# Performance work log

Measured on AMD Instinct MI355X. Metric: run time of the kernel, lower is better.

The kernel has to match this reference:

```python
import jax, jax.numpy as jnp
import numpy as np

D = 768       # input embedding dim
H = 256       # hidden_dim
NH = 4        # num_heads
HD = H // NH  # head_dim = 64
M = 131072    # number of candidate LLM embeddings


def setup_inputs() -> dict:
    key = jax.random.key(0)
    ks = jax.random.split(key, 16)
    s = 0.02
    return {
        "user": jax.random.normal(ks[0], (D,), jnp.float32),
        "query": jax.random.normal(ks[1], (D,), jnp.float32),
        "llm": jax.random.normal(ks[2], (M, D), jnp.float32),
        # projection weights (torch Linear: y = x @ W.T + b)
        "Wu": jax.random.normal(ks[3], (H, D), jnp.float32) * s,
        "bu": jnp.zeros((H,), jnp.float32),
        "Wq": jax.random.normal(ks[4], (H, D), jnp.float32) * s,
        "bq": jnp.zeros((H,), jnp.float32),
        "Wl": jax.random.normal(ks[5], (H, D), jnp.float32) * s,
        "bl": jnp.zeros((H,), jnp.float32),
        # MultiheadAttention packed in-projection [3H, H] and bias [3H]
        "in_proj_w": jax.random.normal(ks[6], (3 * H, H), jnp.float32) * s,
        "in_proj_b": jnp.zeros((3 * H,), jnp.float32),
        "out_proj_w": jax.random.normal(ks[7], (H, H), jnp.float32) * s,
        "out_proj_b": jnp.zeros((H,), jnp.float32),
        # final scoring linear: [1, 2H]
        "Wo": jax.random.normal(ks[8], (1, 2 * H), jnp.float32) * s,
        "bo": jnp.zeros((1,), jnp.float32),
    }


def reference(user, query, llm, Wu, bu, Wq, bq, Wl, bl,
              in_proj_w, in_proj_b, out_proj_w, out_proj_b, Wo, bo):
    m = llm.shape[0]
    # input projections
    u = user @ Wu.T + bu            # [H]
    qv = query @ Wq.T + bq          # [H]
    l = llm @ Wl.T + bl             # [M, H]
    # context rows are identical for every candidate -> compute K/V once on [2, H]
    ctx = jnp.stack([u, qv], axis=0)                      # [2, H]
    Wq_a, Wk_a, Wv_a = jnp.split(in_proj_w, 3, axis=0)    # each [H, H]
    bq_a, bk_a, bv_a = jnp.split(in_proj_b, 3, axis=0)
    q = (l @ Wq_a.T + bq_a).reshape(m, NH, HD)            # [M, nh, hd] (seq_len=1)
    k = (ctx @ Wk_a.T + bk_a).reshape(2, NH, HD)          # [2, nh, hd]
    v = (ctx @ Wv_a.T + bv_a).reshape(2, NH, HD)
    scale = 1.0 / jnp.sqrt(jnp.asarray(HD, q.dtype))
    scores = jnp.einsum('mhd,khd->mhk', q, k) * scale     # [M, nh, 2]
    attn = jax.nn.softmax(scores, axis=-1)
    attended = jnp.einsum('mhk,khd->mhd', attn, v).reshape(m, H)
    attended = attended @ out_proj_w.T + out_proj_b       # [M, H]
    x = jnp.concatenate([attended, l], axis=-1)           # [M, 2H]
    # out = Sequential(ReLU, Dropout(eval=identity), Linear(2H, 1))
    logits = (jax.nn.relu(x) @ Wo.T + bo).squeeze(-1)     # [M]
    return logits
```

## Files before the change

kernel.cpp:

```cpp
#include <hip/hip_runtime.h>


typedef float f32x4 __attribute__((ext_vector_type(4)));
typedef __bf16 bf16x8 __attribute__((ext_vector_type(8)));

#define VMCNT(n) asm volatile("s_waitcnt vmcnt(" #n ")" ::: "memory")

__device__ __forceinline__ unsigned f2bf(float f) {
  unsigned u = __builtin_bit_cast(unsigned, f);
  u += 0x7fffu + ((u >> 16) & 1u);
  return u >> 16;
}

__device__ __forceinline__ void gl_lds16(const void* g, void* l) {
  __builtin_amdgcn_global_load_lds(
      (const __attribute__((address_space(1))) void*)g,
      (__attribute__((address_space(3))) void*)l, 16, 0, 0);
}

__global__ void prep_a(const float* __restrict__ user, const float* __restrict__ query,
                       const float* __restrict__ Wu, const float* __restrict__ bu,
                       const float* __restrict__ Wq, const float* __restrict__ bq,
                       float* __restrict__ wf) {
  const int og = threadIdx.x >> 5, ln = threadIdx.x & 31;
  const int o = blockIdx.x * 8 + og;
  const int isq = o >> 8, j = o & 255;
  const float* Wrow = (isq ? Wq : Wu) + (size_t)j * 768;
  const float* vec = isq ? query : user;
  float p = 0.f;
  #pragma unroll
  for (int i = 0; i < 24; ++i) { int d = ln * 24 + i; p = fmaf(Wrow[d], vec[d], p); }
  #pragma unroll
  for (int off = 16; off; off >>= 1) p += __shfl_xor(p, off);
  if (ln == 0) wf[o] = p + (isq ? bq[j] : bu[j]);
}

__global__ void prep_b(const float* __restrict__ ipw, const float* __restrict__ ipb,
                       float* __restrict__ wf) {
  const int og = threadIdx.x >> 5, ln = threadIdx.x & 31;
  const int o = blockIdx.x * 8 + og;
  const int kv = o >> 9, cc = (o >> 8) & 1, j = o & 255;
  const int row = 256 + kv * 256 + j;
  const float* Wrow = ipw + (size_t)row * 256;
  const float* ctx = wf + cc * 256;
  float p = 0.f;
  #pragma unroll
  for (int i = 0; i < 8; ++i) { int d = ln * 8 + i; p = fmaf(Wrow[d], ctx[d], p); }
  #pragma unroll
  for (int off = 16; off; off >>= 1) p += __shfl_xor(p, off);
  if (ln == 0) wf[512 + o] = p + ipb[row];
}

__global__ void prep_c(const float* __restrict__ ipw, const float* __restrict__ ipb,
                       const float* __restrict__ opw, const float* __restrict__ opb,
                       float* __restrict__ wf) {
  const int t = threadIdx.x, b = blockIdx.x;
  if (b < 4) {
    const int h = b;
    float acc = 0.f;
    for (int d = 0; d < 64; ++d) {
      float kd = wf[512 + h * 64 + d] - wf[768 + h * 64 + d];
      acc = fmaf(ipw[(size_t)(h * 64 + d) * 256 + t], kd, acc);
    }
    wf[1536 + h * 256 + t] = 0.125f * acc;
    if (t == 0) {
      float cs = 0.f;
      for (int d = 0; d < 64; ++d)
        cs = fmaf(ipb[h * 64 + d], wf[512 + h * 64 + d] - wf[768 + h * 64 + d], cs);
      wf[3840 + h] = 0.125f * cs;
    }
  } else {
    const float* oprow = opw + (size_t)t * 256;
    float bse = 0.f;
    for (int i = 0; i < 256; ++i) bse = fmaf(oprow[i], wf[1280 + i], bse);
    wf[2560 + t] = bse + opb[t];
    #pragma unroll
    for (int h = 0; h < 4; ++h) {
      float dl = 0.f;
      for (int d = 0; d < 64; ++d)
        dl = fmaf(oprow[h * 64 + d], wf[1024 + h * 64 + d] - wf[1280 + h * 64 + d], dl);
      wf[2816 + h * 256 + t] = dl;
    }
  }
}

__global__ void prep_w(const float* __restrict__ Wl, unsigned int* __restrict__ Bs4) {
  const int tid = blockIdx.x * 256 + threadIdx.x;
  const int lane = tid & 63;
  const int ntk = tid >> 6;
  const int kk = ntk >> 4, nt = ntk & 15;
  const int k = kk * 32 + (lane >> 4) * 8;
  const int j = nt * 16 + (lane & 15);
  const float* src = Wl + (size_t)j * 768 + k;
  uint4 pk;
  pk.x = f2bf(src[0]) | (f2bf(src[1]) << 16);
  pk.y = f2bf(src[2]) | (f2bf(src[3]) << 16);
  pk.z = f2bf(src[4]) | (f2bf(src[5]) << 16);
  pk.w = f2bf(src[6]) | (f2bf(src[7]) << 16);
  ((uint4*)Bs4)[tid] = pk;
}

__global__ __launch_bounds__(512, 2) void fused_main(
    const float* __restrict__ llm, const float* __restrict__ bl,
    const float* __restrict__ Wo, const float* __restrict__ bo,
    const float* __restrict__ wf, float* __restrict__ out) {

  __shared__ __align__(16) char smem[131072];

  const int t = threadIdx.x;
  const int w = t >> 6, l = t & 63, g = l >> 4, c = l & 15;
  const int wr = w >> 1, wc = w & 1;
  const int m0 = blockIdx.x * 128;
  const char* BsB = (const char*)(wf + 4096);

  auto stage_pair = [&](int slot, int kk) {
    #pragma unroll
    for (int r = 0; r < 2; ++r) {
      const int chunk = r * 512 + w * 64 + l;
      const int row = chunk >> 3;
      const int cb = (chunk & 7) * 16;
      const int cl = cb ^ ((row & 7) << 4);
      const char* gp = (const char*)(llm + (size_t)(m0 + row) * 768 + kk * 32) + cl;
      gl_lds16(gp, smem + slot * 16384 + r * 8192 + w * 1024);
    }
    const char* gb = BsB + (size_t)kk * 16384;
    #pragma unroll
    for (int r = 0; r < 2; ++r) {
      const int chunk = r * 512 + w * 64 + l;
      gl_lds16(gb + (size_t)chunk * 16,
               smem + 65536 + slot * 16384 + r * 8192 + w * 1024);
    }
  };

  stage_pair(0, 0);
  stage_pair(1, 1);
  stage_pair(2, 2);

  f32x4 acc[2][8];
  #pragma unroll
  for (int rf = 0; rf < 2; ++rf)
    #pragma unroll
    for (int cf = 0; cf < 8; ++cf) acc[rf][cf] = (f32x4){0.f, 0.f, 0.f, 0.f};

  const int sx = (c & 7) << 4;

  #pragma unroll
  for (int kk = 0; kk < 24; ++kk) {
    if (kk < 22)      { VMCNT(8); }
    else if (kk == 22){ VMCNT(4); }
    else              { VMCNT(0); }
    __builtin_amdgcn_s_barrier();

    if (kk < 21) stage_pair((kk + 3) & 3, kk + 3);

    const char* ab = smem + (kk & 3) * 16384;
    const char* bb = smem + 65536 + (kk & 3) * 16384 + (size_t)wc * 8192 + l * 16;

    bf16x8 afr[2];
    #pragma unroll
    for (int rf = 0; rf < 2; ++rf) {
      const int row = wr * 32 + rf * 16 + c;
      const char* rp = ab + row * 128;
      const float4 fa = *(const float4*)(rp + ((g * 32) ^ sx));
      const float4 fb = *(const float4*)(rp + ((g * 32 + 16) ^ sx));
      uint4 pk;
      pk.x = f2bf(fa.x) | (f2bf(fa.y) << 16);
      pk.y = f2bf(fa.z) | (f2bf(fa.w) << 16);
      pk.z = f2bf(fb.x) | (f2bf(fb.y) << 16);
      pk.w = f2bf(fb.z) | (f2bf(fb.w) << 16);
      afr[rf] = __builtin_bit_cast(bf16x8, pk);
    }
    #pragma unroll
    for (int cf = 0; cf < 8; ++cf) {
      const bf16x8 bfr = *(const bf16x8*)(bb + cf * 1024);
      #pragma unroll
      for (int rf = 0; rf < 2; ++rf)
        acc[rf][cf] = __builtin_amdgcn_mfma_f32_16x16x32_bf16(
            afr[rf], bfr, acc[rf][cf], 0, 0, 0);
    }
  }

  __syncthreads();

  float* smf = (float*)smem;
  float* wsd_s  = smf;
  float* delta_s = smf + 1024;
  float* base_s = smf + 2048;
  float* woa_s  = smf + 2304;
  float* wo2_s  = smf + 2560;
  float* bl_s   = smf + 2816;
  float* psd_p  = smf + 3072;
  float* pr2_p  = smf + 4096;
  float* a_s    = smf + 4352;
  float* r2_s   = smf + 4864;
  float* p2_s   = smf + 4992;
  float* csd_s  = smf + 5504;
  for (int i = t; i < 1024; i += 512) { wsd_s[i] = wf[1536 + i]; delta_s[i] = wf[2816 + i]; }
  if (t < 256) {
    base_s[t] = wf[2560 + t];
    woa_s[t] = Wo[t];
    wo2_s[t] = Wo[256 + t];
    bl_s[t] = bl[t];
  }
  if (t < 4) csd_s[t] = wf[3840 + t];
  __syncthreads();

  #pragma unroll
  for (int rf = 0; rf < 2; ++rf) {
    float psd[4][4] = {};
    float pr2[4] = {};
    #pragma unroll
    for (int cf = 0; cf < 8; ++cf) {
      const int col = wc * 128 + cf * 16 + c;
      const float w0 = wsd_s[col], w1 = wsd_s[256 + col],
                  w2 = wsd_s[512 + col], w3 = wsd_s[768 + col];
      const float wo = wo2_s[col], bb2 = bl_s[col];
      #pragma unroll
      for (int j = 0; j < 4; ++j) {
        const float x = acc[rf][cf][j] + bb2;
        psd[j][0] = fmaf(x, w0, psd[j][0]);
        psd[j][1] = fmaf(x, w1, psd[j][1]);
        psd[j][2] = fmaf(x, w2, psd[j][2]);
        psd[j][3] = fmaf(x, w3, psd[j][3]);
        pr2[j] = fmaf(fmaxf(x, 0.f), wo, pr2[j]);
      }
    }
    #pragma unroll
    for (int off = 8; off; off >>= 1) {
      #pragma unroll
      for (int j = 0; j < 4; ++j) {
        #pragma unroll
        for (int h = 0; h < 4; ++h) psd[j][h] += __shfl_xor(psd[j][h], off);
        pr2[j] += __shfl_xor(pr2[j], off);
      }
    }
    if (c == 0) {
      #pragma unroll
      for (int j = 0; j < 4; ++j) {
        const int row = wr * 32 + rf * 16 + g * 4 + j;
        #pragma unroll
        for (int h = 0; h < 4; ++h) psd_p[wc * 512 + row * 4 + h] = psd[j][h];
        pr2_p[wc * 128 + row] = pr2[j];
      }
    }
  }
  __syncthreads();

  if (t < 128) {
    #pragma unroll
    for (int h = 0; h < 4; ++h) {
      const float sd = csd_s[h] + psd_p[t * 4 + h] + psd_p[512 + t * 4 + h];
      a_s[t * 4 + h] = 1.f / (1.f + __expf(-sd));
    }
    r2_s[t] = pr2_p[t] + pr2_p[128 + t];
  }
  __syncthreads();

  {
    const int r = t & 127, q = t >> 7;
    const float a0 = a_s[r * 4], a1 = a_s[r * 4 + 1],
                a2 = a_s[r * 4 + 2], a3 = a_s[r * 4 + 3];
    float p = 0.f;
    const int j0 = q * 64;
    #pragma unroll 4
    for (int j = j0; j < j0 + 64; ++j) {
      float att = base_s[j];
      att = fmaf(a0, delta_s[j], att);
      att = fmaf(a1, delta_s[256 + j], att);
      att = fmaf(a2, delta_s[512 + j], att);
      att = fmaf(a3, delta_s[768 + j], att);
      p = fmaf(fmaxf(att, 0.f), woa_s[j], p);
    }
    p2_s[q * 128 + r] = p;
  }
  __syncthreads();
  if (t < 128)
    out[m0 + t] = p2_s[t] + p2_s[128 + t] + p2_s[256 + t] + p2_s[384 + t]
                + r2_s[t] + bo[0];
}

extern "C" void kernel_launch(void* const* d_in, const int* in_sizes, int n_in,
                              void* d_out, int out_size, void* d_ws, size_t ws_size,
                              hipStream_t stream) {
  const float* user  = (const float*)d_in[0];
  const float* query = (const float*)d_in[1];
  const float* llm   = (const float*)d_in[2];
  const float* Wu    = (const float*)d_in[3];
  const float* bu    = (const float*)d_in[4];
  const float* Wq    = (const float*)d_in[5];
  const float* bq    = (const float*)d_in[6];
  const float* Wl    = (const float*)d_in[7];
  const float* bl    = (const float*)d_in[8];
  const float* ipw   = (const float*)d_in[9];
  const float* ipb   = (const float*)d_in[10];
  const float* opw   = (const float*)d_in[11];
  const float* opb   = (const float*)d_in[12];
  const float* Wo    = (const float*)d_in[13];
  const float* bo    = (const float*)d_in[14];
  float* out = (float*)d_out;
  float* wf = (float*)d_ws;
  unsigned int* Bs4 = (unsigned int*)(wf + 4096);

  prep_a<<<64, 256, 0, stream>>>(user, query, Wu, bu, Wq, bq, wf);
  prep_w<<<96, 256, 0, stream>>>(Wl, Bs4);
  prep_b<<<128, 256, 0, stream>>>(ipw, ipb, wf);
  prep_c<<<5, 256, 0, stream>>>(ipw, ipb, opw, opb, wf);
  fused_main<<<131072 / 128, 512, 0, stream>>>(llm, bl, Wo, bo, wf, out);
}
```

Baseline: 197.0 us.

## Merge prep kernels into one launch and shrink main-kernel pipeline to double buffering

Replaces the four small prep kernels with one 97-block kernel. One block computes all the context, K/V and out-projection precomputations serially, passing intermediates through shared memory, while the other blocks convert Wl to bf16. In the main GEMM kernel the 4-stage LDS pipeline becomes a 2-stage double buffer, halving LDS to 64KB so more blocks can be resident per CU. Launch bounds are raised and the k-loop unroll is dropped. The single-block prep does its dot products serially with row-strided loads and may be slow. The shallower pipeline exposes more load latency per block, in exchange for higher occupancy.

```diff
diff --git a/kernel.cpp b/kernel.cpp
--- a/kernel.cpp
+++ b/kernel.cpp
@@ -18,94 +18,86 @@
       (__attribute__((address_space(3))) void*)l, 16, 0, 0);
 }
 
-__global__ void prep_a(const float* __restrict__ user, const float* __restrict__ query,
-                       const float* __restrict__ Wu, const float* __restrict__ bu,
-                       const float* __restrict__ Wq, const float* __restrict__ bq,
-                       float* __restrict__ wf) {
-  const int og = threadIdx.x >> 5, ln = threadIdx.x & 31;
-  const int o = blockIdx.x * 8 + og;
-  const int isq = o >> 8, j = o & 255;
-  const float* Wrow = (isq ? Wq : Wu) + (size_t)j * 768;
-  const float* vec = isq ? query : user;
-  float p = 0.f;
-  #pragma unroll
-  for (int i = 0; i < 24; ++i) { int d = ln * 24 + i; p = fmaf(Wrow[d], vec[d], p); }
-  #pragma unroll
-  for (int off = 16; off; off >>= 1) p += __shfl_xor(p, off);
-  if (ln == 0) wf[o] = p + (isq ? bq[j] : bu[j]);
-}
-
-__global__ void prep_b(const float* __restrict__ ipw, const float* __restrict__ ipb,
-                       float* __restrict__ wf) {
-  const int og = threadIdx.x >> 5, ln = threadIdx.x & 31;
-  const int o = blockIdx.x * 8 + og;
-  const int kv = o >> 9, cc = (o >> 8) & 1, j = o & 255;
-  const int row = 256 + kv * 256 + j;
-  const float* Wrow = ipw + (size_t)row * 256;
-  const float* ctx = wf + cc * 256;
-  float p = 0.f;
-  #pragma unroll
-  for (int i = 0; i < 8; ++i) { int d = ln * 8 + i; p = fmaf(Wrow[d], ctx[d], p); }
-  #pragma unroll
-  for (int off = 16; off; off >>= 1) p += __shfl_xor(p, off);
-  if (ln == 0) wf[512 + o] = p + ipb[row];
-}
-
-__global__ void prep_c(const float* __restrict__ ipw, const float* __restrict__ ipb,
-                       const float* __restrict__ opw, const float* __restrict__ opb,
-                       float* __restrict__ wf) {
-  const int t = threadIdx.x, b = blockIdx.x;
-  if (b < 4) {
-    const int h = b;
+__global__ void prep_all(const float* __restrict__ user, const float* __restrict__ query,
+                         const float* __restrict__ Wu, const float* __restrict__ bu,
+                         const float* __restrict__ Wq, const float* __restrict__ bq,
+                         const float* __restrict__ Wl,
+                         const float* __restrict__ ipw, const float* __restrict__ ipb,
+                         const float* __restrict__ opw, const float* __restrict__ opb,
+                         float* __restrict__ wf, unsigned int* __restrict__ Bs4) {
+  const int t = threadIdx.x;
+  if (blockIdx.x < 96) {
+    const int tid = blockIdx.x * 256 + t;
+    const int lane = tid & 63;
+    const int ntk = tid >> 6;
+    const int kk = ntk >> 4, nt = ntk & 15;
+    const int k = kk * 32 + (lane >> 4) * 8;
+    const int j = nt * 16 + (lane & 15);
+    const float* src = Wl + (size_t)j * 768 + k;
+    uint4 pk;
+    pk.x = f2bf(src[0]) | (f2bf(src[1]) << 16);
+    pk.y = f2bf(src[2]) | (f2bf(src[3]) << 16);
+    pk.z = f2bf(src[4]) | (f2bf(src[5]) << 16);
+    pk.w = f2bf(src[6]) | (f2bf(src[7]) << 16);
+    ((uint4*)Bs4)[tid] = pk;
+    return;
+  }
+  __shared__ float sh[1536];
+  for (int o = t; o < 512; o += 256) {
+    const int isq = o >> 8, j = o & 255;
+    const float* Wrow = (isq ? Wq : Wu) + (size_t)j * 768;
+    const float* vec = isq ? query : user;
+    float p = 0.f;
+    for (int d = 0; d < 768; ++d) p = fmaf(Wrow[d], vec[d], p);
+    p += (isq ? bq[j] : bu[j]);
+    sh[o] = p; wf[o] = p;
+  }
+  __syncthreads();
+  for (int o = t; o < 1024; o += 256) {
+    const int kv = o >> 9, cc = (o >> 8) & 1, j = o & 255;
+    const int row = 256 + kv * 256 + j;
+    const float* Wrow = ipw + (size_t)row * 256;
+    const float* ctx = sh + cc * 256;
+    float p = 0.f;
+    for (int d = 0; d < 256; ++d) p = fmaf(Wrow[d], ctx[d], p);
+    p += ipb[row];
+    sh[512 + o] = p; wf[512 + o] = p;
+  }
+  __syncthreads();
+  #pragma unroll
+  for (int h = 0; h < 4; ++h) {
     float acc = 0.f;
     for (int d = 0; d < 64; ++d) {
-      float kd = wf[512 + h * 64 + d] - wf[768 + h * 64 + d];
+      const float kd = sh[512 + h * 64 + d] - sh[768 + h * 64 + d];
       acc = fmaf(ipw[(size_t)(h * 64 + d) * 256 + t], kd, acc);
     }
     wf[1536 + h * 256 + t] = 0.125f * acc;
-    if (t == 0) {
-      float cs = 0.f;
-      for (int d = 0; d < 64; ++d)
-        cs = fmaf(ipb[h * 64 + d], wf[512 + h * 64 + d] - wf[768 + h * 64 + d], cs);
-      wf[3840 + h] = 0.125f * cs;
-    }
-  } else {
-    const float* oprow = opw + (size_t)t * 256;
-    float bse = 0.f;
-    for (int i = 0; i < 256; ++i) bse = fmaf(oprow[i], wf[1280 + i], bse);
-    wf[2560 + t] = bse + opb[t];
-    #pragma unroll
-    for (int h = 0; h < 4; ++h) {
-      float dl = 0.f;
-      for (int d = 0; d < 64; ++d)
-        dl = fmaf(oprow[h * 64 + d], wf[1024 + h * 64 + d] - wf[1280 + h * 64 + d], dl);
-      wf[2816 + h * 256 + t] = dl;
-    }
-  }
-}
-
-__global__ void prep_w(const float* __restrict__ Wl, unsigned int* __restrict__ Bs4) {
-  const int tid = blockIdx.x * 256 + threadIdx.x;
-  const int lane = tid & 63;
-  const int ntk = tid >> 6;
-  const int kk = ntk >> 4, nt = ntk & 15;
-  const int k = kk * 32 + (lane >> 4) * 8;
-  const int j = nt * 16 + (lane & 15);
-  const float* src = Wl + (size_t)j * 768 + k;
-  uint4 pk;
-  pk.x = f2bf(src[0]) | (f2bf(src[1]) << 16);
-  pk.y = f2bf(src[2]) | (f2bf(src[3]) << 16);
-  pk.z = f2bf(src[4]) | (f2bf(src[5]) << 16);
-  pk.w = f2bf(src[6]) | (f2bf(src[7]) << 16);
-  ((uint4*)Bs4)[tid] = pk;
-}
-
-__global__ __launch_bounds__(512, 2) void fused_main(
+  }
+  if (t < 4) {
+    float cs = 0.f;
+    for (int d = 0; d < 64; ++d)
+      cs = fmaf(ipb[t * 64 + d], sh[512 + t * 64 + d] - sh[768 + t * 64 + d], cs);
+    wf[3840 + t] = 0.125f * cs;
+  }
+  const float* oprow = opw + (size_t)t * 256;
+  float bse = 0.f;
+  for (int i = 0; i < 256; ++i) bse = fmaf(oprow[i], sh[1280 + i], bse);
+  wf[2560 + t] = bse + opb[t];
+  #pragma unroll
+  for (int h = 0; h < 4; ++h) {
+    float dl = 0.f;
+    for (int d = 0; d < 64; ++d)
+      dl = fmaf(oprow[h * 64 + d], sh[1024 + h * 64 + d] - sh[1280 + h * 64 + d], dl);
+    wf[2816 + h * 256 + t] = dl;
+  }
+}
+
+__global__ __launch_bounds__(512, 4) void fused_main(
     const float* __restrict__ llm, const float* __restrict__ bl,
     const float* __restrict__ Wo, const float* __restrict__ bo,
     const float* __restrict__ wf, float* __restrict__ out) {
 
-  __shared__ __align__(16) char smem[131072];
+  __shared__ __align__(16) char smem[65536];
 
   const int t = threadIdx.x;
   const int w = t >> 6, l = t & 63, g = l >> 4, c = l & 15;
@@ -128,13 +120,11 @@
     for (int r = 0; r < 2; ++r) {
       const int chunk = r * 512 + w * 64 + l;
       gl_lds16(gb + (size_t)chunk * 16,
-               smem + 65536 + slot * 16384 + r * 8192 + w * 1024);
+               smem + 32768 + slot * 16384 + r * 8192 + w * 1024);
     }
   };
 
   stage_pair(0, 0);
-  stage_pair(1, 1);
-  stage_pair(2, 2);
 
   f32x4 acc[2][8];
   #pragma unroll
@@ -144,17 +134,13 @@
 
   const int sx = (c & 7) << 4;
 
-  #pragma unroll
   for (int kk = 0; kk < 24; ++kk) {
-    if (kk < 22)      { VMCNT(8); }
-    else if (kk == 22){ VMCNT(4); }
-    else              { VMCNT(0); }
     __builtin_amdgcn_s_barrier();
-
-    if (kk < 21) stage_pair((kk + 3) & 3, kk + 3);
-
-    const char* ab = smem + (kk & 3) * 16384;
-    const char* bb = smem + 65536 + (kk & 3) * 16384 + (size_t)wc * 8192 + l * 16;
+    if (kk < 23) { stage_pair((kk + 1) & 1, kk + 1); VMCNT(4); }
+    else         { VMCNT(0); }
+
+    const char* ab = smem + (kk & 1) * 16384;
+    const char* bb = smem + 32768 + (kk & 1) * 16384 + (size_t)wc * 8192 + l * 16;
 
     bf16x8 afr[2];
     #pragma unroll
@@ -301,9 +287,7 @@
   float* wf = (float*)d_ws;
   unsigned int* Bs4 = (unsigned int*)(wf + 4096);
 
-  prep_a<<<64, 256, 0, stream>>>(user, query, Wu, bu, Wq, bq, wf);
-  prep_w<<<96, 256, 0, stream>>>(Wl, Bs4);
-  prep_b<<<128, 256, 0, stream>>>(ipw, ipb, wf);
-  prep_c<<<5, 256, 0, stream>>>(ipw, ipb, opw, opb, wf);
+  prep_all<<<97, 256, 0, stream>>>(user, query, Wu, bu, Wq, bq, Wl,
+                                   ipw, ipb, opw, opb, wf, Bs4);
   fused_main<<<131072 / 128, 512, 0, stream>>>(llm, bl, Wo, bo, wf, out);
 }
```

New measurement: 258.3 us. +31.1%, slower.
